# Optimization experiments

Measured on AMD Instinct MI355X. Metric: run time of the kernel, lower is better.

Reference implementation:

```python
import jax, jax.numpy as jnp
import numpy as np

B, C, H, W = 4, 64, 128, 128
CQ = C // 8
EPS = 1e-5


def setup_inputs() -> dict:
    key = jax.random.key(0)
    ks = jax.random.split(key, 20)
    r = lambda k, shape, s=0.05: jax.random.normal(k, shape, dtype=jnp.float32) * s
    return {
        "x1": jax.random.normal(ks[0], (B, C, H, W), dtype=jnp.float32),
        "x2": jax.random.normal(ks[1], (B, C, H, W), dtype=jnp.float32),
        # 1x1 convs are plain channel matmuls: weight (out, in), bias (out,)
        "wqA": r(ks[2], (CQ, C)), "bqA": r(ks[3], (CQ,)),
        "wkA": r(ks[4], (CQ, C)), "bkA": r(ks[5], (CQ,)),
        "wvA": r(ks[6], (C, C)),  "bvA": r(ks[7], (C,)),
        "wqB": r(ks[8], (CQ, C)), "bqB": r(ks[9], (CQ,)),
        "wkB": r(ks[10], (CQ, C)), "bkB": r(ks[11], (CQ,)),
        "wvB": r(ks[12], (C, C)),  "bvB": r(ks[13], (C,)),
        "gA": r(ks[14], (1,), 0.1), "gB": r(ks[15], (1,), 0.1),
        "wp": r(ks[16], (C, C)), "bp": r(ks[17], (C,)),
        "bn_g": jnp.ones((C,), dtype=jnp.float32),
        "bn_b": jnp.zeros((C,), dtype=jnp.float32),
    }


def _conv1(x, w, b):
    # 1x1 conv over NCHW == per-pixel channel matmul
    return jnp.einsum('oi,bihw->bohw', w, x) + b[None, :, None, None]


def _axial(q, k, v):
    # criss-cross attention: for each pixel, attend over its row and column,
    # with the column (H) self-position masked to -inf, joint softmax over H+W.
    h = q.shape[2]
    eH = jnp.einsum('bciw,bcjw->biwj', q, k)            # [B,H,W,H] column scores
    eH = jnp.where(jnp.eye(h, dtype=bool)[:, None, :], -jnp.inf, eH)
    eW = jnp.einsum('bchi,bchj->bhij', q, k)            # [B,H,W,W] row scores
    att = jax.nn.softmax(jnp.concatenate([eH, eW], axis=3), axis=3)
    oH = jnp.einsum('bcjw,biwj->bciw', v, att[..., :h])
    oW = jnp.einsum('bchj,bhij->bchi', v, att[..., h:])
    return oH + oW


def _forward(x1, x2, wqA, bqA, wkA, bkA, wvA, bvA, wqB, bqB, wkB, bkB, wvB, bvB,
             gA, gB, wp, bp, bn_g, bn_b):
    # branch A: query from x2, key/value from x1
    out_A = _axial(_conv1(x2, wqA, bqA), _conv1(x1, wkA, bkA), _conv1(x1, wvA, bvA))
    # branch B: query/key/value all from x1
    out_B = _axial(_conv1(x1, wqB, bqB), _conv1(x1, wkB, bkB), _conv1(x1, wvB, bvB))
    diff = jnp.abs(out_A - out_B)
    p = jax.nn.gelu(_conv1(diff, wp, bp), approximate=False)
    # BatchNorm2d in training mode: batch statistics, biased variance
    m = p.mean(axis=(0, 2, 3), keepdims=True)
    v = ((p - m) ** 2).mean(axis=(0, 2, 3), keepdims=True)
    out = (p - m) / jnp.sqrt(v + EPS) * bn_g[None, :, None, None] + bn_b[None, :, None, None]
    return gA[0] * out_A + x1 + out, gB[0] * out_B + x2 + out


def reference(x1, x2, wqA, bqA, wkA, bkA, wvA, bvA, wqB, bqB, wkB, bkB, wvB, bvB,
              gA, gB, wp, bp, bn_g, bn_b):
    return _forward(x1, x2, wqA, bqA, wkA, bkA, wvA, bvA, wqB, bqB, wkB, bkB,
                    wvB, bvB, gA, gB, wp, bp, bn_g, bn_b)
```

## Files before the change

### kernel.cpp

```cpp
#include <hip/hip_runtime.h>


#define NE 4194304ull

typedef __attribute__((ext_vector_type(8))) short short8;
typedef __attribute__((ext_vector_type(4))) float f32x4;
typedef __attribute__((ext_vector_type(16))) float f32x16;

#define HD __device__ __forceinline__

HD float b2f(unsigned short u) { union { unsigned int i; float f; } v; v.i = ((unsigned int)u) << 16; return v.f; }
HD unsigned short f2b(float x) {
  union { float f; unsigned int i; } v; v.f = x;
  unsigned int r = v.i + 0x7FFFu + ((v.i >> 16) & 1u);
  return (unsigned short)(r >> 16);
}
HD unsigned int pk2(float a, float b) {
  return (unsigned int)f2b(a) | ((unsigned int)f2b(b) << 16);
}

HD float erf_fast(float x) {
  const float ax = fabsf(x);
  const float t = 1.0f / (1.0f + 0.3275911f * ax);
  const float poly = ((((1.061405429f*t - 1.453152027f)*t + 1.421413741f)*t
                       - 0.284496736f)*t + 0.254829592f)*t;
  const float y = 1.0f - poly * __expf(-ax*ax);
  return copysignf(y, x);
}

HD unsigned short ldbf(const void* s0, int i, int f) {
  return f ? f2b(((const float*)s0)[i]) : ((const unsigned short*)s0)[i];
}

__global__ __launch_bounds__(256) void prelude_kernel(
    const void* x1,
    const void* wqA, const void* bqA, const void* wkA, const void* bkA,
    const void* wvA, const void* bvA, const void* wqB, const void* bqB,
    const void* wkB, const void* bkB, const void* wvB, const void* bvB,
    const void* wp, const void* bp, const void* gA, const void* gB,
    const void* bng, const void* bnb,
    int* flag, unsigned short* wout)
{
  __shared__ int s;
  if (threadIdx.x == 0) s = 0;
  __syncthreads();
  const float a = fabsf(b2f(((const unsigned short*)x1)[threadIdx.x]));
  if (a > 1000.0f) atomicOr(&s, 1);
  __syncthreads();
  const int f = s;
  if (blockIdx.x == 0 && threadIdx.x == 0) *flag = f;

  const void* srcs[18] = {wqA,bqA,wkA,bkA,wvA,bvA,wqB,bqB,wkB,bkB,wvB,bvB,wp,bp,gA,gB,bng,bnb};
  const int   ns[18]   = {512,  8,512,  8,4096, 64,512,  8,512,  8,4096, 64,4096,64, 1, 1, 64, 64};
  unsigned short* wqkv = wout + 14696;
  float* wbias = (float*)(wout + 25960);

  const int gstride = gridDim.x * 256;
  for (int idx = blockIdx.x*256 + threadIdx.x; idx < 26136; idx += gstride) {
    if (idx < 14690) {
      int off = idx, k2 = 0;
      while (off >= ns[k2]) { off -= ns[k2]; ++k2; }
      wout[idx] = ldbf(srcs[k2], off, f);
    } else if (idx >= 25960) {
      const int i3 = idx - 25960, mt = i3 >> 4, r = i3 & 15;
      float val = 0.0f;
      if (mt == 0)      { if (r < 8) val = b2f(ldbf(bqA, r, f)); }
      else if (mt == 1) { val = b2f((r < 8) ? ldbf(bkA, r, f) : ldbf(bqB, r - 8, f)); }
      else if (mt == 2) { if (r < 8) val = b2f(ldbf(bkB, r, f)); }
      else if (mt < 7)  { val = b2f(ldbf(bvA, (mt-3)*16 + r, f)); }
      else              { val = b2f(ldbf(bvB, (mt-7)*16 + r, f)); }
      wbias[i3] = val;
    } else if (idx >= 14696) {
      const int i2 = idx - 14696;
      const int mt = i2 >> 10, rem = i2 & 1023, r = rem >> 6, ci = rem & 63;
      unsigned short val = 0;
      if (mt == 0)      { if (r < 8) val = ldbf(wqA, r*64 + ci, f); }
      else if (mt == 1) { val = (r < 8) ? ldbf(wkA, r*64 + ci, f) : ldbf(wqB, (r-8)*64 + ci, f); }
      else if (mt == 2) { if (r < 8) val = ldbf(wkB, r*64 + ci, f); }
      else if (mt < 7)  { val = ldbf(wvA, ((mt-3)*16 + r)*64 + ci, f); }
      else              { val = ldbf(wvB, ((mt-7)*16 + r)*64 + ci, f); }
      wqkv[i2] = val;
    }
  }
}

__global__ __launch_bounds__(256) void qkv_kernel(
    const void* __restrict__ x1v, const void* __restrict__ x2v, const int* __restrict__ flag,
    const unsigned short* __restrict__ wqkv, const float* __restrict__ wbias,
    unsigned short* __restrict__ q, unsigned short* __restrict__ k,
    unsigned short* __restrict__ v)
{
  const int hp = blockIdx.x, b = blockIdx.y;
  const int h0 = hp*2;
  const int tid = threadIdx.x, lane = tid & 63, w4 = tid >> 6;
  const int col = lane & 15, quad = lane >> 4;
  const int f32m = *flag;
  __shared__ __align__(16) char smem[33792];
  unsigned short* Xb = (unsigned short*)smem;
  unsigned short* S0 = (unsigned short*)smem;
  unsigned short* S1 = (unsigned short*)(smem + 8448);
  const size_t gb = (size_t)b*1048576 + (size_t)h0*128;

  short8 Bc[2][8];
  #pragma unroll
  for (int pass = 0; pass < 2; ++pass) {
    const void* xv = pass ? x2v : x1v;
    for (int t = tid; t < 2048; t += 256) {
      const int c = t >> 5, rem = t & 31, hh = rem >> 4, w8 = (rem & 15)*8;
      const int n = hh*128 + w8;
      const size_t a = gb + (size_t)c*16384 + (size_t)hh*128 + w8;
      unsigned short vals[8];
      if (f32m) {
        const float* xf = (const float*)xv;
        const float4 f0 = *(const float4*)(xf + a);
        const float4 f1 = *(const float4*)(xf + a + 4);
        vals[0]=f2b(f0.x); vals[1]=f2b(f0.y); vals[2]=f2b(f0.z); vals[3]=f2b(f0.w);
        vals[4]=f2b(f1.x); vals[5]=f2b(f1.y); vals[6]=f2b(f1.z); vals[7]=f2b(f1.w);
      } else {
        const uint4 u = *(const uint4*)((const unsigned short*)xv + a);
        vals[0]=(unsigned short)(u.x & 0xffff); vals[1]=(unsigned short)(u.x >> 16);
        vals[2]=(unsigned short)(u.y & 0xffff); vals[3]=(unsigned short)(u.y >> 16);
        vals[4]=(unsigned short)(u.z & 0xffff); vals[5]=(unsigned short)(u.z >> 16);
        vals[6]=(unsigned short)(u.w & 0xffff); vals[7]=(unsigned short)(u.w >> 16);
      }
      #pragma unroll
      for (int i = 0; i < 8; ++i) Xb[(n + i)*66 + c] = vals[i];
    }
    __syncthreads();
    const unsigned int* U = (const unsigned int*)Xb;
    #pragma unroll
    for (int nt = 0; nt < 4; ++nt)
      #pragma unroll
      for (int ks = 0; ks < 2; ++ks) {
        const int n = w4*64 + nt*16 + col;
        const int base = n*33 + (ks*32 + quad*8)/2;
        union { unsigned int u32[4]; short8 s; } p;
        #pragma unroll
        for (int jj = 0; jj < 4; ++jj) p.u32[jj] = U[base + jj];
        Bc[pass][nt*2 + ks] = p.s;
      }
    __syncthreads();
  }

  #pragma unroll
  for (int mt = 0; mt < 11; ++mt) {
    f32x4 acc[4];
    #pragma unroll
    for (int nt = 0; nt < 4; ++nt) acc[nt] = (f32x4){0.f, 0.f, 0.f, 0.f};
    #pragma unroll
    for (int ks = 0; ks < 2; ++ks) {
      union { uint4 u; short8 s; } A;
      A.u = *(const uint4*)(wqkv + mt*1024 + col*64 + ks*32 + quad*8);
      #pragma unroll
      for (int nt = 0; nt < 4; ++nt)
        acc[nt] = __builtin_amdgcn_mfma_f32_16x16x32_bf16(
            A.s, (mt == 0) ? Bc[1][nt*2 + ks] : Bc[0][nt*2 + ks], acc[nt], 0, 0, 0);
    }
    float bias[4];
    #pragma unroll
    for (int r = 0; r < 4; ++r) bias[r] = wbias[mt*16 + quad*4 + r];
    unsigned short* S = (mt & 1) ? S1 : S0;
    #pragma unroll
    for (int nt = 0; nt < 4; ++nt)
      #pragma unroll
      for (int r = 0; r < 4; ++r) {
        const int row = quad*4 + r;
        const int nloc = w4*64 + nt*16 + col;
        S[row*264 + nloc] = f2b(acc[nt][r] + bias[r]);
      }
    __syncthreads();
    if (mt < 3) {
      const int nloc = tid;
      const int pixg = h0*128 + nloc;
      union { unsigned short u[8]; uint4 v4; } P;
      #pragma unroll
      for (int r = 0; r < 8; ++r) P.u[r] = S[r*264 + nloc];
      if (mt == 0) {
        *(uint4*)(q + ((size_t)b*16384 + pixg)*8) = P.v4;
      } else if (mt == 1) {
        *(uint4*)(k + ((size_t)b*16384 + pixg)*8) = P.v4;
        #pragma unroll
        for (int r = 0; r < 8; ++r) P.u[r] = S[(8 + r)*264 + nloc];
        *(uint4*)(q + ((size_t)(4 + b)*16384 + pixg)*8) = P.v4;
      } else {
        *(uint4*)(k + ((size_t)(4 + b)*16384 + pixg)*8) = P.v4;
      }
    } else {
      const int vm = (mt >= 7) ? mt - 7 : mt - 3;
      const int z  = (mt >= 7) ? 4 + b : b;
      const int cl = tid >> 4, u = tid & 15;
      const int co = vm*16 + cl;
      const uint4 a0 = *(const uint4*)&S[cl*264 + u*16];
      const uint4 a1 = *(const uint4*)&S[cl*264 + u*16 + 8];
      unsigned short* dst = v + ((size_t)(z*64 + co)*16384 + (size_t)h0*128 + u*16);
      *(uint4*)dst = a0;
      *(uint4*)(dst + 8) = a1;
    }
  }
}

__global__ __launch_bounds__(256) void transpose_v(
    const unsigned short* __restrict__ vStd, unsigned short* __restrict__ vT)
{
  const int tile = blockIdx.x, c = blockIdx.y, z = blockIdx.z;
  const int h0 = (tile & 3) * 32, w0 = (tile >> 2) * 32;
  const size_t base = ((size_t)z*64 + c) * 16384;
  __shared__ unsigned short T[32][33];
  const int tid = threadIdx.x;
  for (int idx = tid; idx < 1024; idx += 256) {
    const int r = idx >> 5, cc = idx & 31;
    T[r][cc] = vStd[base + (size_t)(h0 + r)*128 + (w0 + cc)];
  }
  __syncthreads();
  for (int idx = tid; idx < 1024; idx += 256) {
    const int r = idx >> 5, cc = idx & 31;
    vT[base + (size_t)(w0 + r)*128 + (h0 + cc)] = T[cc][r];
  }
}

__global__ __launch_bounds__(256, 4) void pv_kernel(
    const unsigned short* __restrict__ q, const unsigned short* __restrict__ k,
    const unsigned short* __restrict__ vStd, const unsigned short* __restrict__ vT,
    unsigned short* __restrict__ outBrH, unsigned short* __restrict__ oColH,
    float* __restrict__ lRow, float* __restrict__ lCol)
{
  const int X = blockIdx.x, b = blockIdx.y;
  const int br = blockIdx.z & 1, dir = blockIdx.z >> 1;
  const int tid = threadIdx.x, lane = tid & 63, w4 = tid >> 6;
  const int lm = lane & 31, l5 = lane >> 5;
  const int z = br*4 + b;
  const size_t b4h = (size_t)z * 128;
  __shared__ __align__(16) char smem[16384];

  const unsigned short* vsrc = dir ? vStd : vT;
  const size_t vbase = ((size_t)z*64)*16384 + (size_t)X*128;
  for (int t = tid; t < 1024; t += 256) {
    const int c = t >> 4, slot = t & 15;
    const uint4 d = *(const uint4*)(vsrc + vbase + (size_t)c*16384 + slot*8);
    *(uint4*)(smem + c*256 + ((slot*16) ^ ((c & 15) << 4))) = d;
  }

  const uint4 zero4 = {0u, 0u, 0u, 0u};
  short8 qfr;
  {
    union { uint4 u; short8 s; } cv;
    uint4 a = zero4;
    if (l5 == 0) {
      const int m = w4*32 + lm;
      const size_t pix = (b4h + (dir ? X : m))*128 + (dir ? m : X);
      a = *(const uint4*)(q + pix*8);
    }
    cv.u = a; qfr = cv.s;
  }

  float lsum = 0.0f;
  unsigned int pka[4][4], pkb[4][4];
  #pragma unroll
  for (int jt = 0; jt < 4; ++jt) {
    union { uint4 u; short8 s; } kv;
    kv.u = zero4;
    if (l5 == 0) {
      const int j = jt*32 + lm;
      const size_t pix = (b4h + (dir ? X : j))*128 + (dir ? j : X);
      kv.u = *(const uint4*)(k + pix*8);
    }
    f32x16 sacc = (f32x16){0.f,0.f,0.f,0.f,0.f,0.f,0.f,0.f,
                           0.f,0.f,0.f,0.f,0.f,0.f,0.f,0.f};
    sacc = __builtin_amdgcn_mfma_f32_32x32x16_bf16(kv.s, qfr, sacc, 0, 0, 0);
    #pragma unroll
    for (int r2 = 0; r2 < 4; ++r2) {
      float pv4[4];
      #pragma unroll
      for (int e = 0; e < 4; ++e) {
        const int jl = e + 8*r2 + 4*l5;
        float p = 0.0f;
        if (dir || (jt != w4) || (jl != lm)) p = __expf(sacc[r2*4 + e]);
        lsum += p;
        pv4[e] = p;
      }
      pka[jt][r2] = pk2(pv4[0], pv4[1]);
      pkb[jt][r2] = pk2(pv4[2], pv4[3]);
    }
  }

  lsum += __shfl_xor(lsum, 32);
  if (l5 == 0) {
    float* lOut = dir ? lRow : lCol;
    lOut[((size_t)z*128 + X)*128 + w4*32 + lm] = lsum;
  }

  __syncthreads();

  f32x16 acc[2];
  acc[0] = (f32x16){0.f,0.f,0.f,0.f,0.f,0.f,0.f,0.f,0.f,0.f,0.f,0.f,0.f,0.f,0.f,0.f};
  acc[1] = acc[0];
  #pragma unroll
  for (int kb = 0; kb < 8; ++kb) {
    const int qq = kb & 1, jt = kb >> 1;
    const unsigned int ownA = l5 ? pka[jt][2*qq+1] : pka[jt][2*qq];
    const unsigned int ownB = l5 ? pkb[jt][2*qq+1] : pkb[jt][2*qq];
    const unsigned int sndA = l5 ? pka[jt][2*qq]   : pka[jt][2*qq+1];
    const unsigned int sndB = l5 ? pkb[jt][2*qq]   : pkb[jt][2*qq+1];
    const unsigned int rcvA = (unsigned int)__shfl_xor((int)sndA, 32);
    const unsigned int rcvB = (unsigned int)__shfl_xor((int)sndB, 32);
    union { unsigned int u[4]; short8 s; } t4;
    t4.u[0] = l5 ? rcvA : ownA;
    t4.u[1] = l5 ? rcvB : ownB;
    t4.u[2] = l5 ? ownA : rcvA;
    t4.u[3] = l5 ? ownB : rcvB;
    #pragma unroll
    for (int nb = 0; nb < 2; ++nb) {
      const int c = nb*32 + lm;
      union { uint4 u; short8 s; } bv;
      bv.u = *(const uint4*)(smem + c*256 + (((kb*2 + l5)*16) ^ ((c & 15) << 4)));
      acc[nb] = __builtin_amdgcn_mfma_f32_32x32x16_bf16(t4.s, bv.s, acc[nb], 0, 0, 0);
    }
  }

  __syncthreads();

  #pragma unroll
  for (int nb = 0; nb < 2; ++nb) {
    const int c = nb*32 + lm;
    #pragma unroll
    for (int r2 = 0; r2 < 4; ++r2) {
      uint2 u;
      u.x = pk2(acc[nb][r2*4+0], acc[nb][r2*4+1]);
      u.y = pk2(acc[nb][r2*4+2], acc[nb][r2*4+3]);
      const int mbyte = w4*64 + r2*16 + l5*8;
      *(uint2*)(smem + c*256 + (mbyte ^ ((c & 15) << 3))) = u;
    }
  }
  __syncthreads();

  unsigned short* dsth = dir ? outBrH : oColH;
  for (int t = tid; t < 2048; t += 256) {
    const int c = t >> 5, mc = t & 31;
    const uint2 u = *(const uint2*)(smem + c*256 + ((mc*8) ^ ((c & 15) << 3)));
    *(uint2*)(dsth + vbase + (size_t)c*16384 + mc*4) = u;
  }
}

__global__ __launch_bounds__(256) void combine_kernel(
    const unsigned short* __restrict__ oColU, const float* __restrict__ lRow,
    const float* __restrict__ lCol, unsigned short* __restrict__ outBr)
{
  const int tile = blockIdx.x, z = blockIdx.y, cg = blockIdx.z;
  const int h0 = (tile & 3) * 32, w0 = (tile >> 2) * 32, c0 = cg*8;
  const int tid = threadIdx.x;
  __shared__ float Tl[32][33];
  __shared__ __align__(16) float inv[32][36];
  __shared__ __align__(16) float T4[4][32][36];
  const size_t lzb = (size_t)z * 16384;
  {
    const int w = tid >> 3, h4 = (tid & 7)*4;
    const float4 vc = *(const float4*)(lCol + lzb + (size_t)(w0 + w)*128 + h0 + h4);
    Tl[w][h4+0] = vc.x; Tl[w][h4+1] = vc.y; Tl[w][h4+2] = vc.z; Tl[w][h4+3] = vc.w;
  }
  __syncthreads();
  {
    const int h = tid >> 3, w4 = (tid & 7)*4;
    const float4 lr = *(const float4*)(lRow + lzb + (size_t)(h0 + h)*128 + w0 + w4);
    float4 iv;
    iv.x = 1.0f / (lr.x + Tl[w4+0][h]);
    iv.y = 1.0f / (lr.y + Tl[w4+1][h]);
    iv.z = 1.0f / (lr.z + Tl[w4+2][h]);
    iv.w = 1.0f / (lr.w + Tl[w4+3][h]);
    *(float4*)&inv[h][w4] = iv;
  }
  __syncthreads();
  #pragma unroll
  for (int half = 0; half < 2; ++half) {
    for (int t = tid; t < 1024; t += 256) {
      const int ch = t >> 8, rem = t & 255, w = rem >> 3, h4 = (rem & 7)*4;
      const int c = c0 + half*4 + ch;
      const uint2 vc = *(const uint2*)(oColU + ((size_t)(z*64 + c))*16384
                                       + (size_t)(w0 + w)*128 + h0 + h4);
      float4 f;
      f.x = b2f((unsigned short)(vc.x & 0xffff)); f.y = b2f((unsigned short)(vc.x >> 16));
      f.z = b2f((unsigned short)(vc.y & 0xffff)); f.w = b2f((unsigned short)(vc.y >> 16));
      *(float4*)&T4[ch][w][h4] = f;
    }
    __syncthreads();
    for (int t = tid; t < 1024; t += 256) {
      const int ch = t >> 8, rem = t & 255, h = rem >> 3, w4 = (rem & 7)*4;
      const int c = c0 + half*4 + ch;
      const size_t off = ((size_t)(z*64 + c))*16384 + (size_t)(h0 + h)*128 + w0 + w4;
      const uint2 ov = *(const uint2*)(outBr + off);
      const float4 iv = *(const float4*)&inv[h][w4];
      float o0 = b2f((unsigned short)(ov.x & 0xffff));
      float o1 = b2f((unsigned short)(ov.x >> 16));
      float o2 = b2f((unsigned short)(ov.y & 0xffff));
      float o3 = b2f((unsigned short)(ov.y >> 16));
      o0 = (o0 + T4[ch][w4+0][h]) * iv.x;
      o1 = (o1 + T4[ch][w4+1][h]) * iv.y;
      o2 = (o2 + T4[ch][w4+2][h]) * iv.z;
      o3 = (o3 + T4[ch][w4+3][h]) * iv.w;
      uint2 u;
      u.x = (unsigned int)f2b(o0) | ((unsigned int)f2b(o1) << 16);
      u.y = (unsigned int)f2b(o2) | ((unsigned int)f2b(o3) << 16);
      *(uint2*)(outBr + off) = u;
    }
    __syncthreads();
  }
}

__global__ __launch_bounds__(256) void proj_kernel(
    const unsigned short* __restrict__ outA, const unsigned short* __restrict__ outB,
    const unsigned short* __restrict__ wp, const unsigned short* __restrict__ bp,
    unsigned short* __restrict__ pbuf, float* __restrict__ part)
{
  const int hp = blockIdx.x, b = blockIdx.y;
  const int tid = threadIdx.x, lane = tid & 63, w4 = tid >> 6;
  const int col = lane & 15, quad = lane >> 4;
  __shared__ __align__(16) char smem[17408];
  unsigned short* Xb = (unsigned short*)smem;
  float* S = (float*)smem;

  const size_t gb = (size_t)b*1048576 + (size_t)hp*64;
  for (int t = tid; t < 512; t += 256) {
    const int c = t >> 3, rem = t & 7;
    const size_t a = gb + (size_t)c*16384 + rem*8;
    const uint4 ua = *(const uint4*)(outA + a);
    const uint4 ub = *(const uint4*)(outB + a);
    const unsigned short* pa = (const unsigned short*)&ua;
    const unsigned short* pb = (const unsigned short*)&ub;
    const int n = rem*8;
    #pragma unroll
    for (int i = 0; i < 8; ++i)
      Xb[(n + i)*66 + c] = f2b(fabsf(b2f(pa[i]) - b2f(pb[i])));
  }
  __syncthreads();

  short8 Bc[8];
  const unsigned int* U = (const unsigned int*)Xb;
  #pragma unroll
  for (int nt = 0; nt < 4; ++nt)
    #pragma unroll
    for (int ks = 0; ks < 2; ++ks) {
      const int n = nt*16 + col;
      const int base = n*33 + (ks*32 + quad*8)/2;
      union { unsigned int u32[4]; short8 s; } p;
      #pragma unroll
      for (int jj = 0; jj < 4; ++jj) p.u32[jj] = U[base + jj];
      Bc[nt*2 + ks] = p.s;
    }
  __syncthreads();

  f32x4 acc[4];
  #pragma unroll
  for (int nt = 0; nt < 4; ++nt) acc[nt] = (f32x4){0.f, 0.f, 0.f, 0.f};
  #pragma unroll
  for (int ks = 0; ks < 2; ++ks) {
    union { uint4 u; short8 s; } A;
    A.u = *(const uint4*)(wp + (w4*16 + col)*64 + ks*32 + quad*8);
    #pragma unroll
    for (int nt = 0; nt < 4; ++nt)
      acc[nt] = __builtin_amdgcn_mfma_f32_16x16x32_bf16(A.s, Bc[nt*2 + ks], acc[nt], 0, 0, 0);
  }

  float sg1[4] = {0.f, 0.f, 0.f, 0.f}, sg2[4] = {0.f, 0.f, 0.f, 0.f};
  #pragma unroll
  for (int nt = 0; nt < 4; ++nt)
    #pragma unroll
    for (int r = 0; r < 4; ++r) {
      const float x = acc[nt][r] + b2f(bp[w4*16 + quad*4 + r]);
      const float g = 0.5f * x * (1.0f + erf_fast(x * 0.70710678118f));
      S[(w4*16 + quad*4 + r)*68 + nt*16 + col] = g;
      sg1[r] += g; sg2[r] += g*g;
    }
  const int slot = hp*4 + b;
  #pragma unroll
  for (int r = 0; r < 4; ++r) {
    float s1 = sg1[r], s2 = sg2[r];
    s1 += __shfl_xor(s1, 1); s1 += __shfl_xor(s1, 2);
    s1 += __shfl_xor(s1, 4); s1 += __shfl_xor(s1, 8);
    s2 += __shfl_xor(s2, 1); s2 += __shfl_xor(s2, 2);
    s2 += __shfl_xor(s2, 4); s2 += __shfl_xor(s2, 8);
    if (col == 0) {
      const int co = w4*16 + quad*4 + r;
      part[(size_t)co*1024 + slot] = s1;
      part[(size_t)(64 + co)*1024 + slot] = s2;
    }
  }
  __syncthreads();

  for (int t = tid; t < 1024; t += 256) {
    const int row = t >> 4, px4 = (t & 15)*4;
    const float* sp = &S[row*68 + px4];
    uint2 u;
    u.x = pk2(sp[0], sp[1]);
    u.y = pk2(sp[2], sp[3]);
    *(uint2*)(pbuf + (size_t)(b*64 + row)*16384 + hp*64 + px4) = u;
  }
}

__global__ __launch_bounds__(256) void reduce_kernel(
    const float* __restrict__ part, float* __restrict__ bnAcc)
{
  const int stat = blockIdx.x, tid = threadIdx.x;
  const float4 v = *(const float4*)(part + (size_t)stat*1024 + tid*4);
  float s = v.x + v.y + v.z + v.w;
  #pragma unroll
  for (int off = 32; off >= 1; off >>= 1) s += __shfl_xor(s, off);
  __shared__ float ws4[4];
  if ((tid & 63) == 0) ws4[tid >> 6] = s;
  __syncthreads();
  if (tid == 0) bnAcc[stat] = ws4[0] + ws4[1] + ws4[2] + ws4[3];
}

__global__ __launch_bounds__(256) void final_kernel(
    const unsigned short* __restrict__ pbuf,
    const unsigned short* __restrict__ outAH, const unsigned short* __restrict__ outBH,
    const void* __restrict__ x1v, const void* __restrict__ x2v, const int* __restrict__ flag,
    const unsigned short* __restrict__ gA, const unsigned short* __restrict__ gB,
    const unsigned short* __restrict__ bng, const unsigned short* __restrict__ bnb,
    const float* __restrict__ bnAcc, void* __restrict__ outv)
{
  const int f32m = *flag;
  const int idx = (blockIdx.x * 256 + threadIdx.x) * 4;
  const int c = (idx >> 14) & 63;
  const float invN = 1.0f / 65536.0f;
  const float s1 = bnAcc[c], s2 = bnAcc[64 + c];
  const float mean = s1 * invN;
  const float var = s2 * invN - mean*mean;
  const float scale = rsqrtf(var + 1e-5f) * b2f(bng[c]);
  const float beta = b2f(bnb[c]);
  const float ga = b2f(gA[0]), gb = b2f(gB[0]);
  const uint2 uP = *(const uint2*)(pbuf + idx);
  const uint2 uA = *(const uint2*)(outAH + idx);
  const uint2 uB = *(const uint2*)(outBH + idx);
  float p[4] = { b2f((unsigned short)(uP.x & 0xffff)), b2f((unsigned short)(uP.x >> 16)),
                 b2f((unsigned short)(uP.y & 0xffff)), b2f((unsigned short)(uP.y >> 16)) };
  float a[4] = { b2f((unsigned short)(uA.x & 0xffff)), b2f((unsigned short)(uA.x >> 16)),
                 b2f((unsigned short)(uA.y & 0xffff)), b2f((unsigned short)(uA.y >> 16)) };
  float bb[4] = { b2f((unsigned short)(uB.x & 0xffff)), b2f((unsigned short)(uB.x >> 16)),
                  b2f((unsigned short)(uB.y & 0xffff)), b2f((unsigned short)(uB.y >> 16)) };
  float xa[4], xb[4];
  if (f32m) {
    const float4 t1 = *(const float4*)((const float*)x1v + idx);
    const float4 t2 = *(const float4*)((const float*)x2v + idx);
    xa[0]=t1.x; xa[1]=t1.y; xa[2]=t1.z; xa[3]=t1.w;
    xb[0]=t2.x; xb[1]=t2.y; xb[2]=t2.z; xb[3]=t2.w;
  } else {
    const uint2 x1u = *(const uint2*)((const unsigned short*)x1v + idx);
    const uint2 x2u = *(const uint2*)((const unsigned short*)x2v + idx);
    xa[0] = b2f((unsigned short)(x1u.x & 0xffff)); xa[1] = b2f((unsigned short)(x1u.x >> 16));
    xa[2] = b2f((unsigned short)(x1u.y & 0xffff)); xa[3] = b2f((unsigned short)(x1u.y >> 16));
    xb[0] = b2f((unsigned short)(x2u.x & 0xffff)); xb[1] = b2f((unsigned short)(x2u.x >> 16));
    xb[2] = b2f((unsigned short)(x2u.y & 0xffff)); xb[3] = b2f((unsigned short)(x2u.y >> 16));
  }
  float o1f[4], o2f[4];
  #pragma unroll
  for (int t = 0; t < 4; ++t) {
    const float nv = (p[t] - mean)*scale + beta;
    o1f[t] = ga*a[t] + xa[t] + nv;
    o2f[t] = gb*bb[t] + xb[t] + nv;
  }
  if (f32m) {
    float* of = (float*)outv;
    *(float4*)(of + idx)      = (float4){o1f[0], o1f[1], o1f[2], o1f[3]};
    *(float4*)(of + NE + idx) = (float4){o2f[0], o2f[1], o2f[2], o2f[3]};
  } else {
    unsigned short* oh = (unsigned short*)outv;
    uint2 u1, u2;
    u1.x = (unsigned int)f2b(o1f[0]) | ((unsigned int)f2b(o1f[1]) << 16);
    u1.y = (unsigned int)f2b(o1f[2]) | ((unsigned int)f2b(o1f[3]) << 16);
    u2.x = (unsigned int)f2b(o2f[0]) | ((unsigned int)f2b(o2f[1]) << 16);
    u2.y = (unsigned int)f2b(o2f[2]) | ((unsigned int)f2b(o2f[3]) << 16);
    *(uint2*)(oh + idx) = u1;
    *(uint2*)(oh + NE + idx) = u2;
  }
}

extern "C" void kernel_launch(void* const* d_in, const int* in_sizes, int n_in,
                              void* d_out, int out_size, void* d_ws, size_t ws_size,
                              hipStream_t stream)
{
  const void* x1  = d_in[0];
  const void* x2  = d_in[1];

  char* ws = (char*)d_ws;
  const size_t MB = 1048576ull;
  unsigned short* q     = (unsigned short*)(ws);
  unsigned short* kk    = (unsigned short*)(ws + 2*MB);
  float* lRow           = (float*)(ws + 4*MB);
  float* lCol           = (float*)(ws + 4*MB + 512*1024);
  unsigned short* vStd  = (unsigned short*)(ws + 6*MB);
  unsigned short* vT    = (unsigned short*)(ws + 22*MB);
  unsigned short* outBrH= (unsigned short*)(ws + 38*MB);
  unsigned short* oColH = (unsigned short*)(ws + 54*MB);
  unsigned short* pbuf  = (unsigned short*)(ws + 70*MB);
  float* part           = (float*)(ws + 86*MB);
  float* bnAcc          = (float*)(ws + 102*MB);
  int*   flag           = (int*)(ws + 102*MB + 512);
  unsigned short* wC    = (unsigned short*)(ws + 102*MB + 1024);

  prelude_kernel<<<64, 256, 0, stream>>>(
      x1, d_in[2], d_in[3], d_in[4], d_in[5], d_in[6], d_in[7], d_in[8], d_in[9],
      d_in[10], d_in[11], d_in[12], d_in[13], d_in[16], d_in[17], d_in[14], d_in[15],
      d_in[18], d_in[19], flag, wC);
  qkv_kernel<<<dim3(64, 4), 256, 0, stream>>>(
      x1, x2, flag, wC + 14696, (const float*)(wC + 25960), q, kk, vStd);
  transpose_v<<<dim3(16, 64, 8), 256, 0, stream>>>(vStd, vT);
  pv_kernel<<<dim3(128, 4, 4), 256, 0, stream>>>(q, kk, vStd, vT, outBrH, oColH, lRow, lCol);
  combine_kernel<<<dim3(16, 8, 8), 256, 0, stream>>>(oColH, lRow, lCol, outBrH);
  proj_kernel<<<dim3(256, 4), 256, 0, stream>>>(outBrH, outBrH + NE, wC + 10400, wC + 14496, pbuf, part);
  reduce_kernel<<<128, 256, 0, stream>>>(part, bnAcc);
  final_kernel<<<4096, 256, 0, stream>>>(pbuf, outBrH, outBrH + NE, x1, x2, flag,
                                         wC + 14560, wC + 14561, wC + 14562, wC + 14626,
                                         bnAcc, d_out);
}
```

Before: 214.8 us.

## Process four rows per pv_kernel block with batched contiguous V loads

Each pv_kernel block now handles four consecutive X lines instead of one. All four V tiles are loaded into 64KB of shared memory up front using 512-byte contiguous reads per channel, and a separate 16KB staging area holds the output. This is meant to improve load coalescing and amortize per-block setup. In exchange the grid shrinks from 2048 to 512 blocks, shared memory per block grows to 80KB so occupancy falls, and the per-X work runs serially inside each block.

```diff
diff --git a/kernel.cpp b/kernel.cpp
--- a/kernel.cpp
+++ b/kernel.cpp
@@ -218,126 +218,137 @@
   }
 }
 
-__global__ __launch_bounds__(256, 4) void pv_kernel(
+__global__ __launch_bounds__(256) void pv_kernel(
     const unsigned short* __restrict__ q, const unsigned short* __restrict__ k,
     const unsigned short* __restrict__ vStd, const unsigned short* __restrict__ vT,
     unsigned short* __restrict__ outBrH, unsigned short* __restrict__ oColH,
     float* __restrict__ lRow, float* __restrict__ lCol)
 {
-  const int X = blockIdx.x, b = blockIdx.y;
+  const int Xg = blockIdx.x, b = blockIdx.y;
   const int br = blockIdx.z & 1, dir = blockIdx.z >> 1;
   const int tid = threadIdx.x, lane = tid & 63, w4 = tid >> 6;
   const int lm = lane & 31, l5 = lane >> 5;
   const int z = br*4 + b;
   const size_t b4h = (size_t)z * 128;
-  __shared__ __align__(16) char smem[16384];
+  const int X0 = Xg * 4;
+  __shared__ __align__(16) char smem[81920];
+  char* DstB = smem + 65536;
 
   const unsigned short* vsrc = dir ? vStd : vT;
-  const size_t vbase = ((size_t)z*64)*16384 + (size_t)X*128;
-  for (int t = tid; t < 1024; t += 256) {
-    const int c = t >> 4, slot = t & 15;
-    const uint4 d = *(const uint4*)(vsrc + vbase + (size_t)c*16384 + slot*8);
-    *(uint4*)(smem + c*256 + ((slot*16) ^ ((c & 15) << 4))) = d;
-  }
+  const size_t vbase0 = ((size_t)z*64)*16384 + (size_t)X0*128;
+  #pragma unroll
+  for (int it = 0; it < 16; ++it) {
+    const int t = it*256 + tid;
+    const int c = t >> 6, g = t & 63;
+    const uint4 d = *(const uint4*)(vsrc + vbase0 + (size_t)c*16384 + g*8);
+    const int xi = g >> 4, slot = g & 15;
+    *(uint4*)(smem + xi*16384 + c*256 + ((slot*16) ^ ((c & 15) << 4))) = d;
+  }
+  __syncthreads();
 
   const uint4 zero4 = {0u, 0u, 0u, 0u};
-  short8 qfr;
-  {
-    union { uint4 u; short8 s; } cv;
-    uint4 a = zero4;
+  unsigned short* dsth = dir ? outBrH : oColH;
+
+  for (int xi = 0; xi < 4; ++xi) {
+    const int X = X0 + xi;
+    const char* Vb = smem + xi*16384;
+
+    short8 qfr;
+    {
+      union { uint4 u; short8 s; } cv;
+      uint4 a = zero4;
+      if (l5 == 0) {
+        const int m = w4*32 + lm;
+        const size_t pix = (b4h + (dir ? X : m))*128 + (dir ? m : X);
+        a = *(const uint4*)(q + pix*8);
+      }
+      cv.u = a; qfr = cv.s;
+    }
+
+    float lsum = 0.0f;
+    unsigned int pka[4][4], pkb[4][4];
+    #pragma unroll
+    for (int jt = 0; jt < 4; ++jt) {
+      union { uint4 u; short8 s; } kv;
+      kv.u = zero4;
+      if (l5 == 0) {
+        const int j = jt*32 + lm;
+        const size_t pix = (b4h + (dir ? X : j))*128 + (dir ? j : X);
+        kv.u = *(const uint4*)(k + pix*8);
+      }
+      f32x16 sacc = (f32x16){0.f,0.f,0.f,0.f,0.f,0.f,0.f,0.f,
+                             0.f,0.f,0.f,0.f,0.f,0.f,0.f,0.f};
+      sacc = __builtin_amdgcn_mfma_f32_32x32x16_bf16(kv.s, qfr, sacc, 0, 0, 0);
+      #pragma unroll
+      for (int r2 = 0; r2 < 4; ++r2) {
+        float pv4[4];
+        #pragma unroll
+        for (int e = 0; e < 4; ++e) {
+          const int jl = e + 8*r2 + 4*l5;
+          float p = 0.0f;
+          if (dir || (jt != w4) || (jl != lm)) p = __expf(sacc[r2*4 + e]);
+          lsum += p;
+          pv4[e] = p;
+        }
+        pka[jt][r2] = pk2(pv4[0], pv4[1]);
+        pkb[jt][r2] = pk2(pv4[2], pv4[3]);
+      }
+    }
+
+    lsum += __shfl_xor(lsum, 32);
     if (l5 == 0) {
-      const int m = w4*32 + lm;
-      const size_t pix = (b4h + (dir ? X : m))*128 + (dir ? m : X);
-      a = *(const uint4*)(q + pix*8);
-    }
-    cv.u = a; qfr = cv.s;
-  }
-
-  float lsum = 0.0f;
-  unsigned int pka[4][4], pkb[4][4];
-  #pragma unroll
-  for (int jt = 0; jt < 4; ++jt) {
-    union { uint4 u; short8 s; } kv;
-    kv.u = zero4;
-    if (l5 == 0) {
-      const int j = jt*32 + lm;
-      const size_t pix = (b4h + (dir ? X : j))*128 + (dir ? j : X);
-      kv.u = *(const uint4*)(k + pix*8);
-    }
-    f32x16 sacc = (f32x16){0.f,0.f,0.f,0.f,0.f,0.f,0.f,0.f,
-                           0.f,0.f,0.f,0.f,0.f,0.f,0.f,0.f};
-    sacc = __builtin_amdgcn_mfma_f32_32x32x16_bf16(kv.s, qfr, sacc, 0, 0, 0);
-    #pragma unroll
-    for (int r2 = 0; r2 < 4; ++r2) {
-      float pv4[4];
-      #pragma unroll
-      for (int e = 0; e < 4; ++e) {
-        const int jl = e + 8*r2 + 4*l5;
-        float p = 0.0f;
-        if (dir || (jt != w4) || (jl != lm)) p = __expf(sacc[r2*4 + e]);
-        lsum += p;
-        pv4[e] = p;
-      }
-      pka[jt][r2] = pk2(pv4[0], pv4[1]);
-      pkb[jt][r2] = pk2(pv4[2], pv4[3]);
-    }
-  }
-
-  lsum += __shfl_xor(lsum, 32);
-  if (l5 == 0) {
-    float* lOut = dir ? lRow : lCol;
-    lOut[((size_t)z*128 + X)*128 + w4*32 + lm] = lsum;
-  }
-
-  __syncthreads();
-
-  f32x16 acc[2];
-  acc[0] = (f32x16){0.f,0.f,0.f,0.f,0.f,0.f,0.f,0.f,0.f,0.f,0.f,0.f,0.f,0.f,0.f,0.f};
-  acc[1] = acc[0];
-  #pragma unroll
-  for (int kb = 0; kb < 8; ++kb) {
-    const int qq = kb & 1, jt = kb >> 1;
-    const unsigned int ownA = l5 ? pka[jt][2*qq+1] : pka[jt][2*qq];
-    const unsigned int ownB = l5 ? pkb[jt][2*qq+1] : pkb[jt][2*qq];
-    const unsigned int sndA = l5 ? pka[jt][2*qq]   : pka[jt][2*qq+1];
-    const unsigned int sndB = l5 ? pkb[jt][2*qq]   : pkb[jt][2*qq+1];
-    const unsigned int rcvA = (unsigned int)__shfl_xor((int)sndA, 32);
-    const unsigned int rcvB = (unsigned int)__shfl_xor((int)sndB, 32);
-    union { unsigned int u[4]; short8 s; } t4;
-    t4.u[0] = l5 ? rcvA : ownA;
-    t4.u[1] = l5 ? rcvB : ownB;
-    t4.u[2] = l5 ? ownA : rcvA;
-    t4.u[3] = l5 ? ownB : rcvB;
+      float* lOut = dir ? lRow : lCol;
+      lOut[((size_t)z*128 + X)*128 + w4*32 + lm] = lsum;
+    }
+
+    f32x16 acc[2];
+    acc[0] = (f32x16){0.f,0.f,0.f,0.f,0.f,0.f,0.f,0.f,0.f,0.f,0.f,0.f,0.f,0.f,0.f,0.f};
+    acc[1] = acc[0];
+    #pragma unroll
+    for (int kb = 0; kb < 8; ++kb) {
+      const int qq = kb & 1, jt = kb >> 1;
+      const unsigned int ownA = l5 ? pka[jt][2*qq+1] : pka[jt][2*qq];
+      const unsigned int ownB = l5 ? pkb[jt][2*qq+1] : pkb[jt][2*qq];
+      const unsigned int sndA = l5 ? pka[jt][2*qq]   : pka[jt][2*qq+1];
+      const unsigned int sndB = l5 ? pkb[jt][2*qq]   : pkb[jt][2*qq+1];
+      const unsigned int rcvA = (unsigned int)__shfl_xor((int)sndA, 32);
+      const unsigned int rcvB = (unsigned int)__shfl_xor((int)sndB, 32);
+      union { unsigned int u[4]; short8 s; } t4;
+      t4.u[0] = l5 ? rcvA : ownA;
+      t4.u[1] = l5 ? rcvB : ownB;
+      t4.u[2] = l5 ? ownA : rcvA;
+      t4.u[3] = l5 ? ownB : rcvB;
+      #pragma unroll
+      for (int nb = 0; nb < 2; ++nb) {
+        const int c = nb*32 + lm;
+        union { uint4 u; short8 s; } bv;
+        bv.u = *(const uint4*)(Vb + c*256 + (((kb*2 + l5)*16) ^ ((c & 15) << 4)));
+        acc[nb] = __builtin_amdgcn_mfma_f32_32x32x16_bf16(t4.s, bv.s, acc[nb], 0, 0, 0);
+      }
+    }
+
+    __syncthreads();
+
     #pragma unroll
     for (int nb = 0; nb < 2; ++nb) {
       const int c = nb*32 + lm;
-      union { uint4 u; short8 s; } bv;
-      bv.u = *(const uint4*)(smem + c*256 + (((kb*2 + l5)*16) ^ ((c & 15) << 4)));
-      acc[nb] = __builtin_amdgcn_mfma_f32_32x32x16_bf16(t4.s, bv.s, acc[nb], 0, 0, 0);
-    }
-  }
-
-  __syncthreads();
-
-  #pragma unroll
-  for (int nb = 0; nb < 2; ++nb) {
-    const int c = nb*32 + lm;
-    #pragma unroll
-    for (int r2 = 0; r2 < 4; ++r2) {
-      uint2 u;
-      u.x = pk2(acc[nb][r2*4+0], acc[nb][r2*4+1]);
-      u.y = pk2(acc[nb][r2*4+2], acc[nb][r2*4+3]);
-      const int mbyte = w4*64 + r2*16 + l5*8;
-      *(uint2*)(smem + c*256 + (mbyte ^ ((c & 15) << 3))) = u;
-    }
-  }
-  __syncthreads();
-
-  unsigned short* dsth = dir ? outBrH : oColH;
-  for (int t = tid; t < 2048; t += 256) {
-    const int c = t >> 5, mc = t & 31;
-    const uint2 u = *(const uint2*)(smem + c*256 + ((mc*8) ^ ((c & 15) << 3)));
-    *(uint2*)(dsth + vbase + (size_t)c*16384 + mc*4) = u;
+      #pragma unroll
+      for (int r2 = 0; r2 < 4; ++r2) {
+        uint2 u;
+        u.x = pk2(acc[nb][r2*4+0], acc[nb][r2*4+1]);
+        u.y = pk2(acc[nb][r2*4+2], acc[nb][r2*4+3]);
+        const int mbyte = w4*64 + r2*16 + l5*8;
+        *(uint2*)(DstB + c*256 + (mbyte ^ ((c & 15) << 3))) = u;
+      }
+    }
+    __syncthreads();
+
+    const size_t obase = vbase0 + (size_t)xi*128;
+    for (int t = tid; t < 2048; t += 256) {
+      const int c = t >> 5, mc = t & 31;
+      const uint2 u = *(const uint2*)(DstB + c*256 + ((mc*8) ^ ((c & 15) << 3)));
+      *(uint2*)(dsth + obase + (size_t)c*16384 + mc*4) = u;
+    }
   }
 }
 
@@ -603,7 +614,7 @@
   qkv_kernel<<<dim3(64, 4), 256, 0, stream>>>(
       x1, x2, flag, wC + 14696, (const float*)(wC + 25960), q, kk, vStd);
   transpose_v<<<dim3(16, 64, 8), 256, 0, stream>>>(vStd, vT);
-  pv_kernel<<<dim3(128, 4, 4), 256, 0, stream>>>(q, kk, vStd, vT, outBrH, oColH, lRow, lCol);
+  pv_kernel<<<dim3(32, 4, 4), 256, 0, stream>>>(q, kk, vStd, vT, outBrH, oColH, lRow, lCol);
   combine_kernel<<<dim3(16, 8, 8), 256, 0, stream>>>(oColH, lRow, lCol, outBrH);
   proj_kernel<<<dim3(256, 4), 256, 0, stream>>>(outBrH, outBrH + NE, wC + 10400, wC + 14496, pbuf, part);
   reduce_kernel<<<128, 256, 0, stream>>>(part, bnAcc);
```

Result: slower. 222.1 us (+3.4%).
